# Optimization experiments

Measured on AMD Instinct MI355X. Metric: run time of the kernel, lower is better.

Reference implementation:

```python
import jax, jax.numpy as jnp
import numpy as np

SIGMA = 1.0

def setup_inputs() -> dict:
    key = jax.random.key(0)
    k1, k2 = jax.random.split(key)
    N, IN, OUT = 524288, 64, 128
    x = jax.random.normal(k1, (N, IN), dtype=jnp.float32)
    bin_centers = jax.random.normal(k2, (OUT, IN), dtype=jnp.float32)
    return {"x": x, "bin_centers": bin_centers}

def reference(x, bin_centers):
    # distances[n,o] = sum_i (x[n,i] - c[o,i])^2 = ||x_n||^2 - 2 x_n.c_o + ||c_o||^2
    x2 = jnp.sum(x * x, axis=1)[:, None]                # [N,1]
    c2 = jnp.sum(bin_centers * bin_centers, axis=1)[None, :]  # [1,O]
    xc = jnp.einsum('ni,oi->no', x, bin_centers)        # [N,O] GEMM
    distances = x2 - 2.0 * xc + c2                      # [N,O]
    rbf = jnp.exp(-distances / (2.0 * SIGMA ** 2))      # [N,O]
    # histogram[o,i] = sum_n rbf[n,o] * x[n,i]  ->  rbf^T @ x
    histogram = jnp.einsum('no,ni->oi', rbf, x)         # [O,I] GEMM
    return histogram
```

## Files before the change

### kernel.cpp

```cpp
#include <hip/hip_runtime.h>
#include <stdint.h>


typedef _Float16 half8v __attribute__((ext_vector_type(8)));
typedef _Float16 half4v __attribute__((ext_vector_type(4)));
typedef __fp16  fp16x2 __attribute__((ext_vector_type(2)));
typedef float floatx4 __attribute__((ext_vector_type(4)));

#define GRIDN 2048
#define NITER 8
#define LOG2E 1.4426950408889634f
#define PBIAS 38.0f
#define PUNSCALE 3.637978807091713e-12f

#if __has_builtin(__builtin_amdgcn_exp2f)
#define EXP2F(x) __builtin_amdgcn_exp2f(x)
#else
#define EXP2F(x) exp2f(x)
#endif

static __device__ __forceinline__ unsigned int pk16z(float a, float b) {
  fp16x2 h = __builtin_amdgcn_cvt_pkrtz(a, b);
  return __builtin_bit_cast(unsigned int, h);
}
static __device__ __forceinline__ unsigned int pk16(float a, float b) {
  unsigned short ha = __builtin_bit_cast(unsigned short, (_Float16)a);
  unsigned short hb = __builtin_bit_cast(unsigned short, (_Float16)b);
  return (unsigned int)ha | ((unsigned int)hb << 16);
}
static __device__ __forceinline__ half4v mkh4(unsigned int lo, unsigned int hi) {
  uint2 u{lo, hi};
  return __builtin_bit_cast(half4v, u);
}
static __device__ __forceinline__ half8v mkh8(unsigned int a, unsigned int b,
                                              unsigned int c, unsigned int d) {
  uint4 u{a, b, c, d};
  return __builtin_bit_cast(half8v, u);
}

static __device__ __forceinline__ floatx4 mfma32(half8v a, half8v b, floatx4 c) {
  return __builtin_amdgcn_mfma_f32_16x16x32_f16(a, b, c, 0, 0, 0);
}
static __device__ __forceinline__ floatx4 mfma16(half4v a, half4v b, floatx4 c) {
  return __builtin_amdgcn_mfma_f32_16x16x16f16(a, b, c, 0, 0, 0);
}

#define LSTR 72

__global__ __launch_bounds__(256, 4) void rbf_hist_kernel(
    const float* __restrict__ x, const float* __restrict__ c,
    float* __restrict__ out, float* __restrict__ ws, int use_ws) {
  __shared__ unsigned short sXh[32][LSTR];
  __shared__ float          sX2[32];

  const int t    = threadIdx.x;
  const int lane = t & 63;
  const int w    = t >> 6;
  const int l15  = lane & 15;
  const int quad = lane >> 4;

  half8v chi[2][2];
  float m2c[2];
#pragma unroll
  for (int oo = 0; oo < 2; ++oo) {
    const int ot = 2 * w + oo;
    float sq = 0.f;
#pragma unroll
    for (int s = 0; s < 2; ++s) {
      const float* p = c + (ot * 16 + l15) * 64 + s * 32 + quad * 8;
      float4 va = *(const float4*)(p);
      float4 vb = *(const float4*)(p + 4);
      float f[8] = {va.x, va.y, va.z, va.w, vb.x, vb.y, vb.z, vb.w};
      unsigned int h[4];
#pragma unroll
      for (int jp = 0; jp < 4; ++jp) {
        float a = f[2 * jp], b = f[2 * jp + 1];
        sq = fmaf(a, a, sq);
        sq = fmaf(b, b, sq);
        h[jp] = pk16(a * LOG2E, b * LOG2E);
      }
      chi[oo][s] = mkh8(h[0], h[1], h[2], h[3]);
    }
    sq += __shfl_xor(sq, 16);
    sq += __shfl_xor(sq, 32);
    m2c[oo] = fmaf(-0.5f * LOG2E, sq, PBIAS);
  }

  half4v iden;
  {
    float e0 = (quad * 4 + 0 == l15) ? 1.f : 0.f;
    float e1 = (quad * 4 + 1 == l15) ? 1.f : 0.f;
    float e2 = (quad * 4 + 2 == l15) ? 1.f : 0.f;
    float e3 = (quad * 4 + 3 == l15) ? 1.f : 0.f;
    iden = mkh4(pk16z(e0, e1), pk16z(e2, e3));
  }

  floatx4 hacc[2][4];
#pragma unroll
  for (int a = 0; a < 2; ++a)
#pragma unroll
    for (int b = 0; b < 4; ++b) {
      floatx4 z = {0.f, 0.f, 0.f, 0.f};
      hacc[a][b] = z;
    }

  const int r = t >> 3, q = t & 7;
  float4 v[2];
  {
    const float* p = x + ((size_t)blockIdx.x * 32 + r) * 64 + q * 8;
    v[0] = *(const float4*)(p);
    v[1] = *(const float4*)(p + 4);
  }

  for (int it = 0; it < NITER; ++it) {
    __syncthreads();

    {
      float f0 = v[0].x, f1 = v[0].y, f2 = v[0].z, f3 = v[0].w;
      float f4 = v[1].x, f5 = v[1].y, f6 = v[1].z, f7 = v[1].w;
      float sq = 0.f;
      sq = fmaf(f0, f0, sq); sq = fmaf(f1, f1, sq);
      sq = fmaf(f2, f2, sq); sq = fmaf(f3, f3, sq);
      sq = fmaf(f4, f4, sq); sq = fmaf(f5, f5, sq);
      sq = fmaf(f6, f6, sq); sq = fmaf(f7, f7, sq);
      *(uint4*)&sXh[r][q * 8] =
          uint4{pk16(f0, f1), pk16(f2, f3), pk16(f4, f5), pk16(f6, f7)};
      sq += __shfl_xor(sq, 1);
      sq += __shfl_xor(sq, 2);
      sq += __shfl_xor(sq, 4);
      if (q == 0) sX2[r] = -0.5f * LOG2E * sq;
    }
    __syncthreads();

    if (it < NITER - 1) {
      const float* p =
          x + ((size_t)(blockIdx.x + (it + 1) * GRIDN) * 32 + r) * 64 + q * 8;
      v[0] = *(const float4*)(p);
      v[1] = *(const float4*)(p + 4);
    }

#pragma unroll
    for (int t2 = 0; t2 < 2; ++t2) {
      half8v xh0 = *(const half8v*)&sXh[t2 * 16 + l15][quad * 8];
      half8v xh1 = *(const half8v*)&sXh[t2 * 16 + l15][32 + quad * 8];
      float4 m2x = *(const float4*)&sX2[t2 * 16 + quad * 4];

      half4v P[2];
#pragma unroll
      for (int oo = 0; oo < 2; ++oo) {
        floatx4 acc = {m2x.x + m2c[oo], m2x.y + m2c[oo],
                       m2x.z + m2c[oo], m2x.w + m2c[oo]};
        acc = mfma32(xh0, chi[oo][0], acc);
        acc = mfma32(xh1, chi[oo][1], acc);
        P[oo] = mkh4(pk16(EXP2F(acc[0]), EXP2F(acc[1])),
                     pk16(EXP2F(acc[2]), EXP2F(acc[3])));
      }

      half4v XT[4];
#pragma unroll
      for (int itl = 0; itl < 4; ++itl) {
        half4v ax = *(const half4v*)&sXh[t2 * 16 + l15][itl * 16 + quad * 4];
        floatx4 z = {0.f, 0.f, 0.f, 0.f};
        floatx4 d = mfma16(ax, iden, z);
        XT[itl] = mkh4(pk16z(d[0], d[1]), pk16z(d[2], d[3]));
      }

#pragma unroll
      for (int oo = 0; oo < 2; ++oo)
#pragma unroll
        for (int itl = 0; itl < 4; ++itl)
          hacc[oo][itl] = mfma16(P[oo], XT[itl], hacc[oo][itl]);
    }
  }

  if (use_ws) {
    float* part = ws + (size_t)blockIdx.x * 8192;
#pragma unroll
    for (int oo = 0; oo < 2; ++oo)
#pragma unroll
      for (int itl = 0; itl < 4; ++itl)
#pragma unroll
        for (int e = 0; e < 4; ++e) {
          int o = (2 * w + oo) * 16 + quad * 4 + e;
          int i = itl * 16 + l15;
          part[o * 64 + i] = hacc[oo][itl][e] * PUNSCALE;
        }
  } else {
#pragma unroll
    for (int oo = 0; oo < 2; ++oo)
#pragma unroll
      for (int itl = 0; itl < 4; ++itl)
#pragma unroll
        for (int e = 0; e < 4; ++e) {
          int o = (2 * w + oo) * 16 + quad * 4 + e;
          int i = itl * 16 + l15;
          atomicAdd(out + o * 64 + i, hacc[oo][itl][e] * PUNSCALE);
        }
  }
}

__global__ void reduce_kernel(const float* __restrict__ ws, float* __restrict__ out) {
  const int tid = blockIdx.x * 256 + threadIdx.x;
  const int e = tid & 8191;
  const int part = tid >> 13;
  const float* p = ws + (size_t)part * 256 * 8192 + e;
  float s = 0.f;
#pragma unroll 8
  for (int b = 0; b < 256; ++b) s += p[(size_t)b * 8192];
  atomicAdd(out + e, s);
}

__global__ void zero_out_kernel(float* out, int n) {
  int i = blockIdx.x * 256 + threadIdx.x;
  if (i < n) out[i] = 0.f;
}

extern "C" void kernel_launch(void* const* d_in, const int* in_sizes, int n_in,
                              void* d_out, int out_size, void* d_ws, size_t ws_size,
                              hipStream_t stream) {
  (void)in_sizes; (void)n_in;
  const float* x = (const float*)d_in[0];
  const float* c = (const float*)d_in[1];
  float* out = (float*)d_out;
  float* ws  = (float*)d_ws;

  const int use_ws = (ws_size >= (size_t)GRIDN * 8192 * sizeof(float)) ? 1 : 0;

  zero_out_kernel<<<(out_size + 255) / 256, 256, 0, stream>>>(out, out_size);
  rbf_hist_kernel<<<GRIDN, 256, 0, stream>>>(x, c, out, ws, use_ws);
  if (use_ws)
    reduce_kernel<<<256, 256, 0, stream>>>(ws, out);
}
```

Baseline: 217.2 us.

## Halve grid, double per-block iterations, and prefetch two tiles ahead

Halves the grid to 1024 blocks with 16 iterations each and uses two register buffers so global loads of x are issued two tiles ahead instead of one. This hides more memory latency and halves the per-block partial-histogram workspace that the reduce kernel must sum, so the reduce launch is shrunk to 128 blocks. It also switches the exp results to round-toward-zero fp16 packing. The costs are fewer resident blocks to hide latency and more live registers.

```diff
diff --git a/kernel.cpp b/kernel.cpp
--- a/kernel.cpp
+++ b/kernel.cpp
@@ -7,8 +7,8 @@
 typedef __fp16  fp16x2 __attribute__((ext_vector_type(2)));
 typedef float floatx4 __attribute__((ext_vector_type(4)));
 
-#define GRIDN 2048
-#define NITER 8
+#define GRIDN 1024
+#define NITER 16
 #define LOG2E 1.4426950408889634f
 #define PBIAS 38.0f
 #define PUNSCALE 3.637978807091713e-12f
@@ -105,71 +105,83 @@
     }
 
   const int r = t >> 3, q = t & 7;
-  float4 v[2];
+
+  float4 vA[2], vB[2];
   {
-    const float* p = x + ((size_t)blockIdx.x * 32 + r) * 64 + q * 8;
-    v[0] = *(const float4*)(p);
-    v[1] = *(const float4*)(p + 4);
-  }
-
-  for (int it = 0; it < NITER; ++it) {
-    __syncthreads();
-
-    {
-      float f0 = v[0].x, f1 = v[0].y, f2 = v[0].z, f3 = v[0].w;
-      float f4 = v[1].x, f5 = v[1].y, f6 = v[1].z, f7 = v[1].w;
-      float sq = 0.f;
-      sq = fmaf(f0, f0, sq); sq = fmaf(f1, f1, sq);
-      sq = fmaf(f2, f2, sq); sq = fmaf(f3, f3, sq);
-      sq = fmaf(f4, f4, sq); sq = fmaf(f5, f5, sq);
-      sq = fmaf(f6, f6, sq); sq = fmaf(f7, f7, sq);
-      *(uint4*)&sXh[r][q * 8] =
-          uint4{pk16(f0, f1), pk16(f2, f3), pk16(f4, f5), pk16(f6, f7)};
-      sq += __shfl_xor(sq, 1);
-      sq += __shfl_xor(sq, 2);
-      sq += __shfl_xor(sq, 4);
-      if (q == 0) sX2[r] = -0.5f * LOG2E * sq;
-    }
-    __syncthreads();
-
-    if (it < NITER - 1) {
-      const float* p =
-          x + ((size_t)(blockIdx.x + (it + 1) * GRIDN) * 32 + r) * 64 + q * 8;
-      v[0] = *(const float4*)(p);
-      v[1] = *(const float4*)(p + 4);
-    }
-
-#pragma unroll
-    for (int t2 = 0; t2 < 2; ++t2) {
-      half8v xh0 = *(const half8v*)&sXh[t2 * 16 + l15][quad * 8];
-      half8v xh1 = *(const half8v*)&sXh[t2 * 16 + l15][32 + quad * 8];
-      float4 m2x = *(const float4*)&sX2[t2 * 16 + quad * 4];
-
-      half4v P[2];
-#pragma unroll
-      for (int oo = 0; oo < 2; ++oo) {
-        floatx4 acc = {m2x.x + m2c[oo], m2x.y + m2c[oo],
-                       m2x.z + m2c[oo], m2x.w + m2c[oo]};
-        acc = mfma32(xh0, chi[oo][0], acc);
-        acc = mfma32(xh1, chi[oo][1], acc);
-        P[oo] = mkh4(pk16(EXP2F(acc[0]), EXP2F(acc[1])),
-                     pk16(EXP2F(acc[2]), EXP2F(acc[3])));
-      }
-
-      half4v XT[4];
-#pragma unroll
-      for (int itl = 0; itl < 4; ++itl) {
-        half4v ax = *(const half4v*)&sXh[t2 * 16 + l15][itl * 16 + quad * 4];
-        floatx4 z = {0.f, 0.f, 0.f, 0.f};
-        floatx4 d = mfma16(ax, iden, z);
-        XT[itl] = mkh4(pk16z(d[0], d[1]), pk16z(d[2], d[3]));
-      }
-
-#pragma unroll
-      for (int oo = 0; oo < 2; ++oo)
-#pragma unroll
-        for (int itl = 0; itl < 4; ++itl)
-          hacc[oo][itl] = mfma16(P[oo], XT[itl], hacc[oo][itl]);
+    const float* pA = x + ((size_t)blockIdx.x * 32 + r) * 64 + q * 8;
+    vA[0] = *(const float4*)(pA);
+    vA[1] = *(const float4*)(pA + 4);
+    const float* pB =
+        x + ((size_t)(blockIdx.x + GRIDN) * 32 + r) * 64 + q * 8;
+    vB[0] = *(const float4*)(pB);
+    vB[1] = *(const float4*)(pB + 4);
+  }
+
+#pragma unroll 1
+  for (int it = 0; it < NITER; it += 2) {
+#pragma unroll
+    for (int par = 0; par < 2; ++par) {
+      float4* v = (par == 0) ? vA : vB;
+
+      __syncthreads();
+
+      {
+        float f0 = v[0].x, f1 = v[0].y, f2 = v[0].z, f3 = v[0].w;
+        float f4 = v[1].x, f5 = v[1].y, f6 = v[1].z, f7 = v[1].w;
+        float sq = 0.f;
+        sq = fmaf(f0, f0, sq); sq = fmaf(f1, f1, sq);
+        sq = fmaf(f2, f2, sq); sq = fmaf(f3, f3, sq);
+        sq = fmaf(f4, f4, sq); sq = fmaf(f5, f5, sq);
+        sq = fmaf(f6, f6, sq); sq = fmaf(f7, f7, sq);
+        *(uint4*)&sXh[r][q * 8] =
+            uint4{pk16(f0, f1), pk16(f2, f3), pk16(f4, f5), pk16(f6, f7)};
+        sq += __shfl_xor(sq, 1);
+        sq += __shfl_xor(sq, 2);
+        sq += __shfl_xor(sq, 4);
+        if (q == 0) sX2[r] = -0.5f * LOG2E * sq;
+      }
+      __syncthreads();
+
+      if (it + par + 2 < NITER) {
+        const float* p = x +
+            ((size_t)(blockIdx.x + (it + par + 2) * GRIDN) * 32 + r) * 64 +
+            q * 8;
+        v[0] = *(const float4*)(p);
+        v[1] = *(const float4*)(p + 4);
+      }
+
+#pragma unroll
+      for (int t2 = 0; t2 < 2; ++t2) {
+        half8v xh0 = *(const half8v*)&sXh[t2 * 16 + l15][quad * 8];
+        half8v xh1 = *(const half8v*)&sXh[t2 * 16 + l15][32 + quad * 8];
+        float4 m2x = *(const float4*)&sX2[t2 * 16 + quad * 4];
+
+        half4v P[2];
+#pragma unroll
+        for (int oo = 0; oo < 2; ++oo) {
+          floatx4 acc = {m2x.x + m2c[oo], m2x.y + m2c[oo],
+                         m2x.z + m2c[oo], m2x.w + m2c[oo]};
+          acc = mfma32(xh0, chi[oo][0], acc);
+          acc = mfma32(xh1, chi[oo][1], acc);
+          P[oo] = mkh4(pk16z(EXP2F(acc[0]), EXP2F(acc[1])),
+                       pk16z(EXP2F(acc[2]), EXP2F(acc[3])));
+        }
+
+        half4v XT[4];
+#pragma unroll
+        for (int itl = 0; itl < 4; ++itl) {
+          half4v ax = *(const half4v*)&sXh[t2 * 16 + l15][itl * 16 + quad * 4];
+          floatx4 z = {0.f, 0.f, 0.f, 0.f};
+          floatx4 d = mfma16(ax, iden, z);
+          XT[itl] = mkh4(pk16z(d[0], d[1]), pk16z(d[2], d[3]));
+        }
+
+#pragma unroll
+        for (int oo = 0; oo < 2; ++oo)
+#pragma unroll
+          for (int itl = 0; itl < 4; ++itl)
+            hacc[oo][itl] = mfma16(P[oo], XT[itl], hacc[oo][itl]);
+      }
     }
   }
 
@@ -229,5 +241,5 @@
   zero_out_kernel<<<(out_size + 255) / 256, 256, 0, stream>>>(out, out_size);
   rbf_hist_kernel<<<GRIDN, 256, 0, stream>>>(x, c, out, ws, use_ws);
   if (use_ws)
-    reduce_kernel<<<256, 256, 0, stream>>>(ws, out);
-}
+    reduce_kernel<<<128, 256, 0, stream>>>(ws, out);
+}
```

Result: faster. 209.0 us (-3.8%).
